# Performance work log

Measured on AMD Instinct MI355X. Metric: run time of the kernel, lower is better.

The kernel has to match this reference:

```python
import jax, jax.numpy as jnp
import numpy as np

NUM_SYMBOLS = 5
NUM_SUBCARRIERS = 33


def _dft_matrix(n):
    # Unitary DFT matrix: F[j,k] = exp(-2i*pi*j*k/n) / sqrt(n)
    omega = np.exp(-2j * np.pi / n)
    j, k = np.meshgrid(np.arange(n), np.arange(n))
    return (np.power(omega, j * k) / np.sqrt(n)).astype(np.complex64)


def setup_inputs() -> dict:
    key = jax.random.key(0)
    k1, k2 = jax.random.split(key)
    shape = (4096, NUM_SYMBOLS, 4, 4, NUM_SUBCARRIERS)  # (N, S, TXH, TXW, W)
    x_real = jax.random.normal(k1, shape, dtype=jnp.float32)
    x_imag = jax.random.normal(k2, shape, dtype=jnp.float32)
    F_sym = _dft_matrix(NUM_SYMBOLS)
    F_sub = _dft_matrix(NUM_SUBCARRIERS)
    return {
        "x_real": x_real,
        "x_imag": x_imag,
        "F_sym_real": jnp.asarray(F_sym.real, dtype=jnp.float32),
        "F_sym_imag": jnp.asarray(F_sym.imag, dtype=jnp.float32),
        "F_sub_real": jnp.asarray(F_sub.real, dtype=jnp.float32),
        "F_sub_imag": jnp.asarray(F_sub.imag, dtype=jnp.float32),
    }


def reference(x_real, x_imag, F_sym_real, F_sym_imag, F_sub_real, F_sub_imag):
    N, S, TXH, TXW, W = x_real.shape
    x = jax.lax.complex(x_real, x_imag).reshape(N, S, TXH * TXW, W)
    x = jnp.transpose(x, (0, 2, 1, 3))  # (N, A, S, W), A = TXH*TXW

    F_sym = jax.lax.complex(F_sym_real, F_sym_imag)  # (S, S)
    F_sub = jax.lax.complex(F_sub_real, F_sub_imag)  # (W, W)

    # 2D DFT across symbols (left) and subcarriers (right)
    X = jnp.einsum("st,natw->nasw", F_sym, x)
    X = jnp.einsum("nasw,wv->nasv", X, F_sub)

    # magnitude-square (power spectrum)
    X_mag_sq = (X.real * X.real + X.imag * X.imag).astype(jnp.complex64)

    # inverse 2D DFT (conjugate transposes) -> autocorrelation
    X = jnp.einsum("st,natw->nasw", F_sym.conj().T, X_mag_sq)
    X = jnp.einsum("nasw,wv->nasv", X, F_sub.conj().T)

    X = jnp.transpose(X, (0, 2, 1, 3))  # (N, S, A, W)
    return X.reshape(N, S, TXH, TXW, W)
```

## Files before the change

### kernel.cpp

```cpp
#include <hip/hip_runtime.h>

#define NS 5
#define NW 33
#define NA 16
#define SW 165
#define GM 23
#define TPM 11
#define CPT 3
#define THREADS 256
#define ACTIVE (GM*TPM)

__global__ __launch_bounds__(THREADS, 4) void autocorr_kernel(
    const float* __restrict__ x_real, const float* __restrict__ x_imag,
    const float* __restrict__ Fsym_re, const float* __restrict__ Fsym_im,
    const float* __restrict__ Fsub_re, const float* __restrict__ Fsub_im,
    float* __restrict__ out, int NM, int write_complex)
{
    __shared__ float2 sFsym[NS * NS];
    __shared__ float2 sFsub[NW * NW];
    __shared__ float2 buf[GM][SW];

    const int tid = threadIdx.x;
    const int M0 = blockIdx.x * GM;

    for (int i = tid; i < NW * NW; i += THREADS)
        sFsub[i] = make_float2(Fsub_re[i], Fsub_im[i]);
    if (tid < NS * NS) sFsym[tid] = make_float2(Fsym_re[tid], Fsym_im[tid]);

    for (int e = tid; e < GM * SW; e += THREADS) {
        int g = e / SW, r = e % SW;
        int t = r / NW, w = r % NW;
        int M = M0 + g;
        float2 val = make_float2(0.f, 0.f);
        if (M < NM) {
            int n = M >> 4, a = M & 15;
            int off = ((n * NS + t) * NA + a) * NW + w;
            val = make_float2(x_real[off], x_imag[off]);
        }
        buf[g][w * NS + t] = val;
    }
    __syncthreads();

    const int g = tid / TPM;
    const int j = tid - g * TPM;
    const bool act = (tid < ACTIVE);
    const int M = M0 + g;
    const int c0 = 3 * j;

    float2 V[NS][CPT];
#pragma unroll
    for (int t = 0; t < NS; ++t)
#pragma unroll
        for (int k = 0; k < CPT; ++k) V[t][k] = make_float2(0.f, 0.f);
    if (act) {
        const float2* bp = buf[g];
#pragma unroll 3
        for (int w = 0; w < NW; ++w) {
            float2 xc[NS];
#pragma unroll
            for (int t = 0; t < NS; ++t) xc[t] = bp[w * NS + t];
            float2 fv[CPT];
#pragma unroll
            for (int k = 0; k < CPT; ++k) fv[k] = sFsub[w * NW + c0 + k];
#pragma unroll
            for (int t = 0; t < NS; ++t)
#pragma unroll
                for (int k = 0; k < CPT; ++k) {
                    V[t][k].x = fmaf(xc[t].x, fv[k].x, V[t][k].x);
                    V[t][k].x = fmaf(-xc[t].y, fv[k].y, V[t][k].x);
                    V[t][k].y = fmaf(xc[t].x, fv[k].y, V[t][k].y);
                    V[t][k].y = fmaf(xc[t].y, fv[k].x, V[t][k].y);
                }
        }
    }

    float2 T2[3][CPT];
#pragma unroll
    for (int p = 0; p < 3; ++p)
#pragma unroll
        for (int k = 0; k < CPT; ++k) T2[p][k] = make_float2(0.f, 0.f);
    if (act) {
#pragma unroll
        for (int s = 0; s < NS; ++s) {
            float2 X[CPT];
#pragma unroll
            for (int k = 0; k < CPT; ++k) X[k] = make_float2(0.f, 0.f);
#pragma unroll
            for (int t = 0; t < NS; ++t) {
                float2 f = sFsym[s * NS + t];
#pragma unroll
                for (int k = 0; k < CPT; ++k) {
                    X[k].x = fmaf(f.x, V[t][k].x, X[k].x);
                    X[k].x = fmaf(-f.y, V[t][k].y, X[k].x);
                    X[k].y = fmaf(f.x, V[t][k].y, X[k].y);
                    X[k].y = fmaf(f.y, V[t][k].x, X[k].y);
                }
            }
            float P[CPT];
#pragma unroll
            for (int k = 0; k < CPT; ++k)
                P[k] = X[k].x * X[k].x + X[k].y * X[k].y;
#pragma unroll
            for (int p = 0; p < 3; ++p) {
                float2 f = sFsym[s * NS + p];
#pragma unroll
                for (int k = 0; k < CPT; ++k) {
                    T2[p][k].x = fmaf(f.x, P[k], T2[p][k].x);
                    T2[p][k].y = fmaf(-f.y, P[k], T2[p][k].y);
                }
            }
        }
    }
    __syncthreads();

    if (act) {
#pragma unroll
        for (int k = 0; k < CPT; ++k)
#pragma unroll
            for (int p = 0; p < 3; ++p)
                buf[g][(c0 + k) * 3 + p] = T2[p][k];
    }
    __syncthreads();

    if (act) {
        const float2* bp = buf[g];
        if (!write_complex) {
            float Yr[3][CPT];
#pragma unroll
            for (int p = 0; p < 3; ++p)
#pragma unroll
                for (int k = 0; k < CPT; ++k) Yr[p][k] = 0.f;
#pragma unroll 3
            for (int v = 0; v < NW; ++v) {
                float2 tc[3];
#pragma unroll
                for (int p = 0; p < 3; ++p) tc[p] = bp[v * 3 + p];
                float2 fw[CPT];
#pragma unroll
                for (int k = 0; k < CPT; ++k) fw[k] = sFsub[(c0 + k) * NW + v];
#pragma unroll
                for (int p = 0; p < 3; ++p)
#pragma unroll
                    for (int k = 0; k < CPT; ++k) {
                        Yr[p][k] = fmaf(tc[p].x, fw[k].x, Yr[p][k]);
                        Yr[p][k] = fmaf(tc[p].y, fw[k].y, Yr[p][k]);
                    }
            }
            if (M < NM) {
                int n = M >> 4, a = M & 15;
                int obase = ((n * NS) * NA + a) * NW;
#pragma unroll
                for (int p = 0; p < 3; ++p) {
                    const int pp = (NS - p) % NS;
#pragma unroll
                    for (int k = 0; k < CPT; ++k) {
                        const int q = c0 + k;
                        const int qq = (NW - q) % NW;
                        out[obase + p * (NA * NW) + q] = Yr[p][k];
                        out[obase + pp * (NA * NW) + qq] = Yr[p][k];
                    }
                }
            }
        } else {
            float2 Y[3][CPT];
#pragma unroll
            for (int p = 0; p < 3; ++p)
#pragma unroll
                for (int k = 0; k < CPT; ++k) Y[p][k] = make_float2(0.f, 0.f);
            for (int v = 0; v < NW; ++v) {
                float2 tc[3];
#pragma unroll
                for (int p = 0; p < 3; ++p) tc[p] = bp[v * 3 + p];
                float2 fw[CPT];
#pragma unroll
                for (int k = 0; k < CPT; ++k) fw[k] = sFsub[(c0 + k) * NW + v];
#pragma unroll
                for (int p = 0; p < 3; ++p)
#pragma unroll
                    for (int k = 0; k < CPT; ++k) {
                        Y[p][k].x = fmaf(tc[p].x, fw[k].x, Y[p][k].x);
                        Y[p][k].x = fmaf(tc[p].y, fw[k].y, Y[p][k].x);
                        Y[p][k].y = fmaf(tc[p].y, fw[k].x, Y[p][k].y);
                        Y[p][k].y = fmaf(-tc[p].x, fw[k].y, Y[p][k].y);
                    }
            }
            if (M < NM) {
                int n = M >> 4, a = M & 15;
#pragma unroll
                for (int p = 0; p < 3; ++p) {
                    const int pp = (NS - p) % NS;
#pragma unroll
                    for (int k = 0; k < CPT; ++k) {
                        const int q = c0 + k;
                        const int qq = (NW - q) % NW;
                        ((float2*)out)[((n * NS + p) * NA + a) * NW + q] = Y[p][k];
                        ((float2*)out)[((n * NS + pp) * NA + a) * NW + qq] =
                            make_float2(Y[p][k].x, -Y[p][k].y);
                    }
                }
            }
        }
    }
}

extern "C" void kernel_launch(void* const* d_in, const int* in_sizes, int n_in,
                              void* d_out, int out_size, void* d_ws, size_t ws_size,
                              hipStream_t stream) {
    const float* x_real  = (const float*)d_in[0];
    const float* x_imag  = (const float*)d_in[1];
    const float* Fsym_re = (const float*)d_in[2];
    const float* Fsym_im = (const float*)d_in[3];
    const float* Fsub_re = (const float*)d_in[4];
    const float* Fsub_im = (const float*)d_in[5];

    const int NM = in_sizes[0] / SW;
    const long long n_cplx = (long long)in_sizes[0];
    const int write_complex = ((long long)out_size >= 2 * n_cplx) ? 1 : 0;

    const int blocks = (NM + GM - 1) / GM;

    autocorr_kernel<<<blocks, THREADS, 0, stream>>>(
        x_real, x_imag, Fsym_re, Fsym_im, Fsub_re, Fsub_im,
        (float*)d_out, NM, write_complex);
}
```

Baseline: 191.8 us.

## Partition block work per wavefront to replace block barriers with wave-local sync

Each 64-lane wavefront now owns 5 matrices (20 per block) with its own slice of the shared buffer. It loads that slice, computes on it and writes it back itself, so the block-wide __syncthreads after the load and around the intermediate store become s_waitcnt lgkmcnt(0) waits. This removes block-level stalls and lets waves overlap global loads with compute independently. The trade-off is that only 55 of 64 lanes do work, fewer matrices are handled per block, and correctness now relies on lockstep execution within a wave for LDS visibility.

```diff
diff --git a/kernel.cpp b/kernel.cpp
--- a/kernel.cpp
+++ b/kernel.cpp
@@ -4,11 +4,11 @@
 #define NW 33
 #define NA 16
 #define SW 165
-#define GM 23
+#define MPW 5
+#define GM 20
 #define TPM 11
 #define CPT 3
 #define THREADS 256
-#define ACTIVE (GM*TPM)
 
 __global__ __launch_bounds__(THREADS, 4) void autocorr_kernel(
     const float* __restrict__ x_real, const float* __restrict__ x_imag,
@@ -21,30 +21,36 @@
     __shared__ float2 buf[GM][SW];
 
     const int tid = threadIdx.x;
-    const int M0 = blockIdx.x * GM;
 
     for (int i = tid; i < NW * NW; i += THREADS)
         sFsub[i] = make_float2(Fsub_re[i], Fsub_im[i]);
     if (tid < NS * NS) sFsym[tid] = make_float2(Fsym_re[tid], Fsym_im[tid]);
-
-    for (int e = tid; e < GM * SW; e += THREADS) {
-        int g = e / SW, r = e % SW;
-        int t = r / NW, w = r % NW;
-        int M = M0 + g;
+    __syncthreads();
+
+    const int wave = tid >> 6;
+    const int lane = tid & 63;
+    const int Mw = blockIdx.x * GM + wave * MPW;
+    float2* const wbuf = &buf[wave * MPW][0];
+
+    for (int e = lane; e < MPW * SW; e += 64) {
+        const int g = e / SW, r = e - g * SW;
+        const int t = r / NW, w = r - t * NW;
+        const int M = Mw + g;
         float2 val = make_float2(0.f, 0.f);
         if (M < NM) {
-            int n = M >> 4, a = M & 15;
-            int off = ((n * NS + t) * NA + a) * NW + w;
+            const int n = M >> 4, a = M & 15;
+            const int off = ((n * NS + t) * NA + a) * NW + w;
             val = make_float2(x_real[off], x_imag[off]);
         }
-        buf[g][w * NS + t] = val;
-    }
-    __syncthreads();
-
-    const int g = tid / TPM;
-    const int j = tid - g * TPM;
-    const bool act = (tid < ACTIVE);
-    const int M = M0 + g;
+        wbuf[g * SW + w * NS + t] = val;
+    }
+    asm volatile("s_waitcnt lgkmcnt(0)" ::: "memory");
+
+    const int g = lane / TPM;
+    const int j = lane - g * TPM;
+    const bool act = (lane < MPW * TPM);
+    const int gg = act ? g : 0;
+    const int M = Mw + g;
     const int c0 = 3 * j;
 
     float2 V[NS][CPT];
@@ -53,7 +59,7 @@
 #pragma unroll
         for (int k = 0; k < CPT; ++k) V[t][k] = make_float2(0.f, 0.f);
     if (act) {
-        const float2* bp = buf[g];
+        const float2* bp = wbuf + gg * SW;
 #pragma unroll 3
         for (int w = 0; w < NW; ++w) {
             float2 xc[NS];
@@ -110,20 +116,16 @@
                 }
             }
         }
-    }
-    __syncthreads();
+#pragma unroll
+        for (int k = 0; k < CPT; ++k)
+#pragma unroll
+            for (int p = 0; p < 3; ++p)
+                wbuf[gg * SW + (c0 + k) * 3 + p] = T2[p][k];
+    }
+    asm volatile("s_waitcnt lgkmcnt(0)" ::: "memory");
 
     if (act) {
-#pragma unroll
-        for (int k = 0; k < CPT; ++k)
-#pragma unroll
-            for (int p = 0; p < 3; ++p)
-                buf[g][(c0 + k) * 3 + p] = T2[p][k];
-    }
-    __syncthreads();
-
-    if (act) {
-        const float2* bp = buf[g];
+        const float2* bp = wbuf + gg * SW;
         if (!write_complex) {
             float Yr[3][CPT];
 #pragma unroll
```

Result: no change. 190.2 us (-0.8%).
